# Optimization experiments

Measured on AMD Instinct MI355X. Metric: run time of the kernel, lower is better.

Reference implementation:

```python
import jax, jax.numpy as jnp
import numpy as np

V = 100000  # vocabulary_size
E = 128     # embedding_dimension
B = 2048    # batch size


def setup_inputs() -> dict:
    key = jax.random.key(0)
    k1, k2, k3, k4, k5 = jax.random.split(key, 5)
    center_word = jax.random.randint(k1, (B,), 0, V, dtype=jnp.int64)
    # nn.Linear(V, E): weight [E, V], bias [E]
    W_center = jax.random.normal(k2, (E, V), dtype=jnp.float32) * 0.02
    b_center = jax.random.normal(k3, (E,), dtype=jnp.float32) * 0.02
    # nn.Linear(E, V): weight [V, E], bias [V]
    W_out = jax.random.normal(k4, (V, E), dtype=jnp.float32) * 0.02
    b_out = jax.random.normal(k5, (V,), dtype=jnp.float32) * 0.02
    return {"center_word": center_word, "W_center": W_center,
            "b_center": b_center, "W_out": W_out, "b_out": b_out}


def reference(center_word, W_center, b_center, W_out, b_out):
    # one-hot @ W_center.T == gather of W_center columns (faithful, no O(V) matmul)
    emb = W_center.T[center_word] + b_center          # [B, E]
    logits = emb @ W_out.T + b_out                    # [B, V]
    return jax.nn.log_softmax(logits, axis=1)
```

## Files before the change

kernel.cpp:

```cpp
#include <hip/hip_runtime.h>
#include <hip/hip_bf16.h>

#define VV 100000
#define EE 128
#define BB 2048
#define BM 128
#define BN 128
#define LDK 136
#define NWG (((VV + BN - 1) / BN) * (BB / BM))

typedef __bf16 bf16x8 __attribute__((ext_vector_type(8)));
typedef float  f32x4  __attribute__((ext_vector_type(4)));

__device__ __forceinline__ unsigned short f2bf(float f) {
    union { float f; unsigned u; } x; x.f = f;
    unsigned r = x.u + 0x7fffu + ((x.u >> 16) & 1u);
    return (unsigned short)(r >> 16);
}

__global__ __launch_bounds__(256) void prep_kernel(
    const int* __restrict__ idx, const float* __restrict__ Wc,
    const float* __restrict__ bc, unsigned short* __restrict__ embB,
    float* __restrict__ s)
{
    int gid = blockIdx.x * 256 + threadIdx.x;
    int b = gid >> 7, e = gid & 127;
    float v = Wc[(size_t)e * VV + idx[b]] + bc[e];
    embB[gid] = f2bf(v);
    if (gid < BB) s[gid] = 0.0f;
}

__global__ __launch_bounds__(256) void lse_kernel(
    const float* __restrict__ s, float* __restrict__ lse)
{
    int gid = blockIdx.x * 256 + threadIdx.x;
    if (gid < BB) lse[gid] = logf(s[gid]);
}

template <int PASS>
__global__ __launch_bounds__(256, 4) void gemm_kernel(
    const unsigned short* __restrict__ embB,
    const float*  __restrict__ Wout,
    const float*  __restrict__ bout,
    float* __restrict__ sumexp,
    const float* __restrict__ lse,
    float* __restrict__ out)
{
    __shared__ unsigned short sB[BN * LDK];
    __shared__ float sSum[BM];

    const int tid = threadIdx.x;
    const int bid   = blockIdx.y * gridDim.x + blockIdx.x;
    const int wgid  = (bid & 7) * (NWG / 8) + (bid >> 3);
    const int rbase = (wgid & 15) * BM;
    const int vbase = (wgid >> 4) * BN;

    if (PASS == 1 && tid < BM) sSum[tid] = 0.0f;

    #pragma unroll
    for (int it = 0; it < 16; ++it) {
        int k4 = tid + it * 256;
        int row = k4 >> 5, c4 = k4 & 31;
        int v = vbase + row;
        float4 w = make_float4(0.f, 0.f, 0.f, 0.f);
        if (v < VV) w = *(const float4*)(Wout + (size_t)v * EE + c4 * 4);
        ushort4 h;
        h.x = f2bf(w.x); h.y = f2bf(w.y); h.z = f2bf(w.z); h.w = f2bf(w.w);
        *(ushort4*)(sB + row * LDK + c4 * 4) = h;
    }
    __syncthreads();

    const int lane = tid & 63;
    const int wave = tid >> 6;
    const int wr   = (wave >> 1) * 64;
    const int wc   = (wave & 1) * 64;
    const int l16  = lane & 15;
    const int quad = lane >> 4;

    f32x4 acc[4][4];
    #pragma unroll
    for (int i = 0; i < 4; ++i)
        #pragma unroll
        for (int j = 0; j < 4; ++j)
            acc[i][j] = (f32x4){0.f, 0.f, 0.f, 0.f};

    #pragma unroll
    for (int ks = 0; ks < 4; ++ks) {
        bf16x8 a[4], b[4];
        #pragma unroll
        for (int i = 0; i < 4; ++i)
            a[i] = *(const bf16x8*)(embB + (size_t)(rbase + wr + i * 16 + l16) * EE
                                         + ks * 32 + quad * 8);
        #pragma unroll
        for (int j = 0; j < 4; ++j)
            b[j] = *(const bf16x8*)(sB + (wc + j * 16 + l16) * LDK + ks * 32 + quad * 8);
        #pragma unroll
        for (int i = 0; i < 4; ++i)
            #pragma unroll
            for (int j = 0; j < 4; ++j)
                acc[i][j] = __builtin_amdgcn_mfma_f32_16x16x32_bf16(a[i], b[j], acc[i][j], 0, 0, 0);
    }

    if (PASS == 1) {
        #pragma unroll
        for (int i = 0; i < 4; ++i) {
            float rs[4] = {0.f, 0.f, 0.f, 0.f};
            #pragma unroll
            for (int j = 0; j < 4; ++j) {
                int v = vbase + wc + j * 16 + l16;
                if (v < VV) {
                    float bo = bout[v];
                    #pragma unroll
                    for (int r = 0; r < 4; ++r)
                        rs[r] += __expf(acc[i][j][r] + bo);
                }
            }
            #pragma unroll
            for (int r = 0; r < 4; ++r) {
                float t = rs[r];
                t += __shfl_xor(t, 1);
                t += __shfl_xor(t, 2);
                t += __shfl_xor(t, 4);
                t += __shfl_xor(t, 8);
                if (l16 == 0)
                    atomicAdd(&sSum[wr + i * 16 + quad * 4 + r], t);
            }
        }
        __syncthreads();
        if (tid < BM) atomicAdd(&sumexp[rbase + tid], sSum[tid]);
    } else {
        #pragma unroll
        for (int i = 0; i < 4; ++i) {
            int row0 = rbase + wr + i * 16 + quad * 4;
            #pragma unroll
            for (int r = 0; r < 4; ++r) {
                float l = lse[row0 + r];
                #pragma unroll
                for (int j = 0; j < 4; ++j) {
                    int v = vbase + wc + j * 16 + l16;
                    if (v < VV)
                        out[(size_t)(row0 + r) * VV + v] = acc[i][j][r] + bout[v] - l;
                }
            }
        }
    }
}

extern "C" void kernel_launch(void* const* d_in, const int* in_sizes, int n_in,
                              void* d_out, int out_size, void* d_ws, size_t ws_size,
                              hipStream_t stream) {
    const int*   idx  = (const int*)d_in[0];
    const float* Wc   = (const float*)d_in[1];
    const float* bc   = (const float*)d_in[2];
    const float* Wout = (const float*)d_in[3];
    const float* bout = (const float*)d_in[4];
    float* out = (float*)d_out;

    unsigned short* embB = (unsigned short*)d_ws;
    float* s   = (float*)((char*)d_ws + BB * EE * sizeof(unsigned short));
    float* lse = (float*)((char*)s + BB * sizeof(float));

    prep_kernel<<<(BB * EE) / 256, 256, 0, stream>>>(idx, Wc, bc, embB, s);

    dim3 grid(BB / BM, (VV + BN - 1) / BN);
    gemm_kernel<1><<<grid, 256, 0, stream>>>(embB, Wout, bout, s, nullptr, nullptr);
    lse_kernel<<<(BB + 255) / 256, 256, 0, stream>>>(s, lse);
    gemm_kernel<2><<<grid, 256, 0, stream>>>(embB, Wout, bout, nullptr, lse, out);
}
```

Before: 1.354 ms.

## Pre-convert W_out to bf16, load tiles via direct-to-LDS with XOR swizzle, vectorize epilogue

Adds a one-time kernel that converts W_out to bf16 in workspace, so each GEMM tile can be loaded with global_load_lds straight into an XOR-swizzled LDS layout instead of converting fp32 in registers in every workgroup of both passes. The MFMA operands are swapped so each lane holds four consecutive vocab columns. This lets the output pass store float4 and load bias as float4, and lets the sum-exp pass reduce with two shuffles and direct global atomics instead of an LDS staging array. It also raises the occupancy hint to 5. It costs an extra W_out conversion pass and depends on the workspace being large enough, with the old path kept as a fallback.

```diff
diff --git a/kernel.cpp b/kernel.cpp
--- a/kernel.cpp
+++ b/kernel.cpp
@@ -6,7 +6,6 @@
 #define BB 2048
 #define BM 128
 #define BN 128
-#define LDK 136
 #define NWG (((VV + BN - 1) / BN) * (BB / BM))
 
 typedef __bf16 bf16x8 __attribute__((ext_vector_type(8)));
@@ -16,6 +15,12 @@
     union { float f; unsigned u; } x; x.f = f;
     unsigned r = x.u + 0x7fffu + ((x.u >> 16) & 1u);
     return (unsigned short)(r >> 16);
+}
+
+__device__ __forceinline__ void gload_lds16(const void* g, void* l) {
+    __builtin_amdgcn_global_load_lds(
+        (const __attribute__((address_space(1))) void*)g,
+        (__attribute__((address_space(3))) void*)l, 16, 0, 0);
 }
 
 __global__ __launch_bounds__(256) void prep_kernel(
@@ -30,6 +35,20 @@
     if (gid < BB) s[gid] = 0.0f;
 }
 
+__global__ __launch_bounds__(256) void wconv_kernel(
+    const float* __restrict__ W, unsigned short* __restrict__ Wb)
+{
+    int gid = blockIdx.x * 256 + threadIdx.x;
+    const float4* src = (const float4*)W + (size_t)gid * 2;
+    float4 w0 = src[0], w1 = src[1];
+    int4 o;
+    o.x = f2bf(w0.x) | (f2bf(w0.y) << 16);
+    o.y = f2bf(w0.z) | (f2bf(w0.w) << 16);
+    o.z = f2bf(w1.x) | (f2bf(w1.y) << 16);
+    o.w = f2bf(w1.z) | (f2bf(w1.w) << 16);
+    *(int4*)(Wb + (size_t)gid * 8) = o;
+}
+
 __global__ __launch_bounds__(256) void lse_kernel(
     const float* __restrict__ s, float* __restrict__ lse)
 {
@@ -37,45 +56,59 @@
     if (gid < BB) lse[gid] = logf(s[gid]);
 }
 
-template <int PASS>
-__global__ __launch_bounds__(256, 4) void gemm_kernel(
+template <int PASS, int PRE>
+__global__ __launch_bounds__(256, 5) void gemm_kernel(
     const unsigned short* __restrict__ embB,
     const float*  __restrict__ Wout,
+    const unsigned short* __restrict__ WoutB,
     const float*  __restrict__ bout,
     float* __restrict__ sumexp,
     const float* __restrict__ lse,
     float* __restrict__ out)
 {
-    __shared__ unsigned short sB[BN * LDK];
-    __shared__ float sSum[BM];
-
-    const int tid = threadIdx.x;
+    __shared__ __align__(16) unsigned short sB[BN * 128];
+
+    const int tid  = threadIdx.x;
+    const int lane = tid & 63;
+    const int wave = tid >> 6;
+
     const int bid   = blockIdx.y * gridDim.x + blockIdx.x;
     const int wgid  = (bid & 7) * (NWG / 8) + (bid >> 3);
     const int rbase = (wgid & 15) * BM;
     const int vbase = (wgid >> 4) * BN;
 
-    if (PASS == 1 && tid < BM) sSum[tid] = 0.0f;
-
-    #pragma unroll
-    for (int it = 0; it < 16; ++it) {
-        int k4 = tid + it * 256;
-        int row = k4 >> 5, c4 = k4 & 31;
-        int v = vbase + row;
-        float4 w = make_float4(0.f, 0.f, 0.f, 0.f);
-        if (v < VV) w = *(const float4*)(Wout + (size_t)v * EE + c4 * 4);
-        ushort4 h;
-        h.x = f2bf(w.x); h.y = f2bf(w.y); h.z = f2bf(w.z); h.w = f2bf(w.w);
-        *(ushort4*)(sB + row * LDK + c4 * 4) = h;
+    if (PRE) {
+        const int lrow = lane >> 4;
+        const int lcol = (lane & 15) << 4;
+        #pragma unroll
+        for (int it = 0; it < 8; ++it) {
+            int r  = it * 16 + wave * 4 + lrow;
+            int vr = vbase + r; if (vr > VV - 1) vr = VV - 1;
+            const char* g = (const char*)WoutB + (size_t)vr * 256
+                          + (lcol ^ ((r & 7) << 4));
+            char* l = (char*)sB + (it * 16 + wave * 4) * 256;
+            gload_lds16(g, l);
+        }
+    } else {
+        #pragma unroll
+        for (int it = 0; it < 16; ++it) {
+            int k4 = tid + it * 256;
+            int row = k4 >> 5, c4 = k4 & 31;
+            int v = vbase + row;
+            float4 w = make_float4(0.f, 0.f, 0.f, 0.f);
+            if (v < VV) w = *(const float4*)(Wout + (size_t)v * EE + c4 * 4);
+            int2 h;
+            h.x = f2bf(w.x) | (f2bf(w.y) << 16);
+            h.y = f2bf(w.z) | (f2bf(w.w) << 16);
+            *(int2*)((char*)sB + row * 256 + ((c4 * 8) ^ ((row & 7) << 4))) = h;
+        }
     }
     __syncthreads();
 
-    const int lane = tid & 63;
-    const int wave = tid >> 6;
+    const int l16  = lane & 15;
+    const int quad = lane >> 4;
     const int wr   = (wave >> 1) * 64;
     const int wc   = (wave & 1) * 64;
-    const int l16  = lane & 15;
-    const int quad = lane >> 4;
 
     f32x4 acc[4][4];
     #pragma unroll
@@ -92,54 +125,57 @@
             a[i] = *(const bf16x8*)(embB + (size_t)(rbase + wr + i * 16 + l16) * EE
                                          + ks * 32 + quad * 8);
         #pragma unroll
-        for (int j = 0; j < 4; ++j)
-            b[j] = *(const bf16x8*)(sB + (wc + j * 16 + l16) * LDK + ks * 32 + quad * 8);
+        for (int j = 0; j < 4; ++j) {
+            int row = wc + j * 16 + l16;
+            b[j] = *(const bf16x8*)((const char*)sB + row * 256
+                                    + ((ks * 64 + quad * 16) ^ ((row & 7) << 4)));
+        }
         #pragma unroll
         for (int i = 0; i < 4; ++i)
             #pragma unroll
             for (int j = 0; j < 4; ++j)
-                acc[i][j] = __builtin_amdgcn_mfma_f32_16x16x32_bf16(a[i], b[j], acc[i][j], 0, 0, 0);
+                acc[i][j] = __builtin_amdgcn_mfma_f32_16x16x32_bf16(b[j], a[i], acc[i][j], 0, 0, 0);
     }
 
     if (PASS == 1) {
         #pragma unroll
         for (int i = 0; i < 4; ++i) {
-            float rs[4] = {0.f, 0.f, 0.f, 0.f};
+            float t = 0.f;
             #pragma unroll
             for (int j = 0; j < 4; ++j) {
-                int v = vbase + wc + j * 16 + l16;
-                if (v < VV) {
-                    float bo = bout[v];
-                    #pragma unroll
-                    for (int r = 0; r < 4; ++r)
-                        rs[r] += __expf(acc[i][j][r] + bo);
+                int v0 = vbase + wc + j * 16 + quad * 4;
+                if (v0 < VV) {
+                    float4 bo = *(const float4*)(bout + v0);
+                    t += __expf(acc[i][j][0] + bo.x);
+                    t += __expf(acc[i][j][1] + bo.y);
+                    t += __expf(acc[i][j][2] + bo.z);
+                    t += __expf(acc[i][j][3] + bo.w);
                 }
             }
-            #pragma unroll
-            for (int r = 0; r < 4; ++r) {
-                float t = rs[r];
-                t += __shfl_xor(t, 1);
-                t += __shfl_xor(t, 2);
-                t += __shfl_xor(t, 4);
-                t += __shfl_xor(t, 8);
-                if (l16 == 0)
-                    atomicAdd(&sSum[wr + i * 16 + quad * 4 + r], t);
-            }
-        }
-        __syncthreads();
-        if (tid < BM) atomicAdd(&sumexp[rbase + tid], sSum[tid]);
+            t += __shfl_xor(t, 16);
+            t += __shfl_xor(t, 32);
+            if (lane < 16)
+                atomicAdd(&sumexp[rbase + wr + i * 16 + lane], t);
+        }
     } else {
-        #pragma unroll
-        for (int i = 0; i < 4; ++i) {
-            int row0 = rbase + wr + i * 16 + quad * 4;
-            #pragma unroll
-            for (int r = 0; r < 4; ++r) {
-                float l = lse[row0 + r];
+        float l[4];
+        #pragma unroll
+        for (int i = 0; i < 4; ++i)
+            l[i] = lse[rbase + wr + i * 16 + l16];
+        #pragma unroll
+        for (int j = 0; j < 4; ++j) {
+            int v0 = vbase + wc + j * 16 + quad * 4;
+            if (v0 < VV) {
+                float4 bo = *(const float4*)(bout + v0);
                 #pragma unroll
-                for (int j = 0; j < 4; ++j) {
-                    int v = vbase + wc + j * 16 + l16;
-                    if (v < VV)
-                        out[(size_t)(row0 + r) * VV + v] = acc[i][j][r] + bout[v] - l;
+                for (int i = 0; i < 4; ++i) {
+                    int m = rbase + wr + i * 16 + l16;
+                    float4 st;
+                    st.x = acc[i][j][0] + bo.x - l[i];
+                    st.y = acc[i][j][1] + bo.y - l[i];
+                    st.z = acc[i][j][2] + bo.z - l[i];
+                    st.w = acc[i][j][3] + bo.w - l[i];
+                    *(float4*)(out + (size_t)m * VV + v0) = st;
                 }
             }
         }
@@ -159,11 +195,22 @@
     unsigned short* embB = (unsigned short*)d_ws;
     float* s   = (float*)((char*)d_ws + BB * EE * sizeof(unsigned short));
     float* lse = (float*)((char*)s + BB * sizeof(float));
+    unsigned short* WoutB = (unsigned short*)((char*)lse + BB * sizeof(float));
+    const size_t need = (size_t)BB * EE * 2 + 2 * BB * 4 + (size_t)VV * EE * 2;
+    const bool pre = ws_size >= need;
 
     prep_kernel<<<(BB * EE) / 256, 256, 0, stream>>>(idx, Wc, bc, embB, s);
+    if (pre)
+        wconv_kernel<<<(VV * EE / 8) / 256, 256, 0, stream>>>(Wout, WoutB);
 
     dim3 grid(BB / BM, (VV + BN - 1) / BN);
-    gemm_kernel<1><<<grid, 256, 0, stream>>>(embB, Wout, bout, s, nullptr, nullptr);
-    lse_kernel<<<(BB + 255) / 256, 256, 0, stream>>>(s, lse);
-    gemm_kernel<2><<<grid, 256, 0, stream>>>(embB, Wout, bout, nullptr, lse, out);
-}
+    if (pre) {
+        gemm_kernel<1, 1><<<grid, 256, 0, stream>>>(embB, Wout, WoutB, bout, s, nullptr, nullptr);
+        lse_kernel<<<(BB + 255) / 256, 256, 0, stream>>>(s, lse);
+        gemm_kernel<2, 1><<<grid, 256, 0, stream>>>(embB, Wout, WoutB, bout, nullptr, lse, out);
+    } else {
+        gemm_kernel<1, 0><<<grid, 256, 0, stream>>>(embB, Wout, WoutB, bout, s, nullptr, nullptr);
+        lse_kernel<<<(BB + 255) / 256, 256, 0, stream>>>(s, lse);
+        gemm_kernel<2, 0><<<grid, 256, 0, stream>>>(embB, Wout, WoutB, bout, nullptr, lse, out);
+    }
+}
```

New measurement: 1.511 ms. 1.12x slower.
